# Performance work log

Measured on AMD Instinct MI355X. Metric: run time of the kernel, lower is better.

## Reference

```python
import jax, jax.numpy as jnp
import numpy as np

H = 256  # GRU hidden size


def _gru_scan(state, lengths, Wih, Whh, bih, bhh):
    # state: [B, T, D]; run a batched GRU over time, freezing h once t >= lengths[b]
    B, T, D = state.shape
    # precompute input gates for all timesteps: [T, B, 3H]
    gi_all = jnp.einsum('btd,gd->tbg', state, Wih) + bih

    def step(h, inp):
        gi, t = inp
        gh = h @ Whh.T + bhh                       # [B, 3H]
        i_r, i_z, i_n = jnp.split(gi, 3, axis=-1)
        h_r, h_z, h_n = jnp.split(gh, 3, axis=-1)
        r = jax.nn.sigmoid(i_r + h_r)
        z = jax.nn.sigmoid(i_z + h_z)
        n = jnp.tanh(i_n + r * h_n)
        h_new = (1.0 - z) * n + z * h              # torch GRUCell update
        mask = (t < lengths)[:, None]              # ragged: stop updating past length
        return jnp.where(mask, h_new, h), None

    h0 = jnp.zeros((B, H), state.dtype)
    h, _ = jax.lax.scan(step, h0, (gi_all, jnp.arange(T)))
    return h  # [B, H] = hidden after lengths[b] GRU steps


def _mlp(x, w1, b1, w2, b2, w3, b3, w4, b4, wq, bq):
    x = jax.nn.relu(x @ w1.T + b1)
    x = jax.nn.relu(x @ w2.T + b2)
    x = jax.nn.relu(x @ w3.T + b3)
    x = jax.nn.relu(x @ w4.T + b4)
    return x @ wq.T + bq  # [B, 1]


def setup_inputs() -> dict:
    key = jax.random.key(0)
    ks = jax.random.split(key, 40)
    B, T, D, A = 2048, 64, 15, 1
    inp = {}
    inp['state'] = jax.random.normal(ks[0], (B, T, D), jnp.float32)
    inp['action'] = jax.random.normal(ks[1], (B, A), jnp.float32)
    inp['lengths'] = jax.random.randint(ks[2], (B,), 1, T + 1, jnp.int32)
    i = 3
    for t in (1, 2):
        for name, shape, fan in [('Wih', (3 * H, D), D), ('Whh', (3 * H, H), H),
                                 ('bih', (3 * H,), H), ('bhh', (3 * H,), H)]:
            inp[f'g{t}_{name}'] = jax.random.normal(ks[i], shape, jnp.float32) / np.sqrt(fan)
            i += 1
        for name, (o, n) in [('fc1', (1024, H + D + A)), ('fc2', (1024, 1024)),
                             ('fc3', (512, 1024)), ('fc4', (256, 512)), ('q', (1, 256))]:
            inp[f'{name}_{t}_w'] = jax.random.normal(ks[i], (o, n), jnp.float32) / np.sqrt(n)
            i += 1
            inp[f'{name}_{t}_b'] = jax.random.normal(ks[i], (o,), jnp.float32) * 0.01
            i += 1
    return inp


def reference(state, action, lengths,
              g1_Wih, g1_Whh, g1_bih, g1_bhh,
              fc1_1_w, fc1_1_b, fc2_1_w, fc2_1_b, fc3_1_w, fc3_1_b,
              fc4_1_w, fc4_1_b, q_1_w, q_1_b,
              g2_Wih, g2_Whh, g2_bih, g2_bhh,
              fc1_2_w, fc1_2_b, fc2_2_w, fc2_2_b, fc3_2_w, fc3_2_b,
              fc4_2_w, fc4_2_b, q_2_w, q_2_b):
    h1 = _gru_scan(state, lengths, g1_Wih, g1_Whh, g1_bih, g1_bhh)
    h2 = _gru_scan(state, lengths, g2_Wih, g2_Whh, g2_bih, g2_bhh)
    aug = jnp.concatenate([state[:, 0, :], action], axis=-1)  # [B, 16]
    x1 = jnp.concatenate([aug, h1], axis=-1)                  # [B, 272]
    x2 = jnp.concatenate([aug, h2], axis=-1)
    out1 = _mlp(x1, fc1_1_w, fc1_1_b, fc2_1_w, fc2_1_b, fc3_1_w, fc3_1_b,
                fc4_1_w, fc4_1_b, q_1_w, q_1_b)
    out2 = _mlp(x2, fc1_2_w, fc1_2_b, fc2_2_w, fc2_2_b, fc3_2_w, fc3_2_b,
                fc4_2_w, fc4_2_b, q_2_w, q_2_b)
    return (out1, out2)
```

## Files before the change

kernel.cpp:

```cpp
#include <hip/hip_runtime.h>

typedef float  f32x4 __attribute__((ext_vector_type(4)));
typedef short  s16x8 __attribute__((ext_vector_type(8)));
typedef __bf16 b16x8 __attribute__((ext_vector_type(8)));

#define DEV __device__ __forceinline__

DEV unsigned short f2b(float f) {
  unsigned u = __builtin_bit_cast(unsigned, f);
  u = (u + 0x7FFFu + ((u >> 16) & 1u)) >> 16;
  return (unsigned short)u;
}
DEV b16x8 ld8(const unsigned short* p) {
  return __builtin_bit_cast(b16x8, *(const s16x8*)p);
}
DEV float sigm(float x) { return __builtin_amdgcn_rcpf(1.f + __expf(-x)); }
DEV float tanh_fast(float x) {
  float e = __expf(2.f * x);
  return 1.f - 2.f * __builtin_amdgcn_rcpf(e + 1.f);
}
DEV f32x4 mfma_bf16(b16x8 a, b16x8 b, f32x4 c) {
  return __builtin_amdgcn_mfma_f32_16x16x32_bf16(a, b, c, 0, 0, 0);
}

struct PrepArgs {
  const float *whh[2], *wih[2], *bih[2], *bhh[2];
  const float *src[2][4];
  unsigned short *waug[2], *dst[2][4];
  const float *qb[2];
  float *out;
};

__global__ __launch_bounds__(256) void prep_kernel(PrepArgs p) {
  const int job = blockIdx.y;
  const int i0 = blockIdx.x * 256 + threadIdx.x;
  const int stride = gridDim.x * 256;
  if (job < 2) {
    const float* whh = p.whh[job];
    const float* wih = p.wih[job];
    const float* bih = p.bih[job];
    const float* bhh = p.bhh[job];
    unsigned short* dst = p.waug[job];
    for (int idx = i0; idx < 768 * 288; idx += stride) {
      int j = idx / 288, k = idx - j * 288;
      float v = 0.f;
      if (k < 256) {
        int o = k & 31;
        int kk = (k & 0x1E0) + (o >> 1) + ((o & 1) << 4);
        v = whh[j * 256 + kk];
      } else if (k < 271)  v = wih[j * 15 + (k - 256)];
      else if (k == 271)   v = (j < 512) ? (bih[j] + bhh[j]) : bih[j];
      dst[idx] = f2b(v);
    }
  } else if (job < 10) {
    const int jj = job - 2, br = jj >> 2, ly = jj & 3;
    const int rowsA[4] = {1024, 1024, 512, 256};
    const int scA[4]   = {272, 1024, 1024, 512};
    const int dcA[4]   = {320, 1024, 1024, 512};
    const float* src = p.src[br][ly];
    unsigned short* dst = p.dst[br][ly];
    const int sc = scA[ly], dc = dcA[ly], tot = rowsA[ly] * dc;
    for (int idx = i0; idx < tot; idx += stride) {
      int r = idx / dc, c = idx - r * dc;
      float v = (c < sc) ? src[r * sc + c] : 0.f;
      dst[idx] = f2b(v);
    }
  } else {
    for (int idx = i0; idx < 4096; idx += stride)
      p.out[idx] = p.qb[idx >> 11][0];
  }
}

#define GRU_LDS_BYTES 147584
__attribute__((amdgpu_waves_per_eu(1, 1)))
__global__ void __launch_bounds__(256) gru_kernel(
    const float* __restrict__ state, const float* __restrict__ action,
    const int* __restrict__ lengths,
    const unsigned short* __restrict__ waug0, const unsigned short* __restrict__ waug1,
    const float* __restrict__ bhh0, const float* __restrict__ bhh1,
    unsigned short* __restrict__ x0, unsigned short* __restrict__ x1) {
  extern __shared__ char smem[];
  unsigned short* W7   = (unsigned short*)smem;
  unsigned short* WA   = (unsigned short*)(smem + 49152);
  unsigned short* SgL  = (unsigned short*)(smem + 98304);
  unsigned*       Hb2  = (unsigned*)(smem + 131072);
  int* lenS = (int*)(smem + 147456);
  int* mlS  = (int*)(smem + 147520);

  const int tid = threadIdx.x;
  const int lane = tid & 63, w = tid >> 6;
  const int l15 = lane & 15, q = lane >> 4;
  const int g = blockIdx.x & 1;
  const int r0 = (blockIdx.x >> 1) * 16;

  const unsigned short* Waug = g ? waug1 : waug0;
  const float* bhh = g ? bhh1 : bhh0;
  unsigned short* xout = g ? x1 : x0;

  for (int i = tid; i < 4096; i += 256) Hb2[i] = 0;
  if (tid < 16) lenS[tid] = lengths[r0 + tid];
  for (int s = tid; s < 64 * 32; s += 256) {
    const int t = s >> 5, L = s & 31;
    const int q2 = L >> 4, r = L & 15;
    const float* sp = state + (size_t)(r0 + r) * 960 + t * 15;
    s16x8 h;
#pragma unroll
    for (int j = 0; j < 8; j++) {
      const int k = q2 * 8 + j;
      float v = (k < 15) ? sp[k] : (k == 15 ? 1.0f : 0.f);
      h[j] = (short)f2b(v);
    }
    *(s16x8*)(SgL + (size_t)s * 8) = h;
  }
  __syncthreads();
  if (tid == 0) {
    int m = 1;
    for (int i = 0; i < 16; i++) m = lenS[i] > m ? lenS[i] : m;
    *mlS = m;
  }

  int c0[12];
#pragma unroll
  for (int gate = 0; gate < 3; gate++)
#pragma unroll
    for (int j = 0; j < 4; j++) c0[gate * 4 + j] = gate * 256 + 64 * w + 16 * j;

  b16x8 wres[12][7];
#pragma unroll
  for (int i = 0; i < 12; i++) {
    const unsigned short* bpi = Waug + (size_t)(c0[i] + l15) * 288 + q * 8;
#pragma unroll
    for (int j = 0; j < 7; j++) wres[i][j] = ld8(bpi + j * 32);
    *(s16x8*)(W7 + ((size_t)i * 256 + tid) * 8) =
        __builtin_bit_cast(s16x8, ld8(bpi + 7 * 32));
    *(s16x8*)(WA + ((size_t)i * 256 + tid) * 8) =
        __builtin_bit_cast(s16x8, ld8(bpi + 256));
  }
  float bnH[4];
#pragma unroll
  for (int j = 0; j < 4; j++) bnH[j] = bhh[c0[8 + j] + l15];
  int len4[4];
#pragma unroll
  for (int r = 0; r < 4; r++) len4[r] = lenS[q * 4 + r];

  int aOff[8];
#pragma unroll
  for (int k = 0; k < 8; k++) {
    const int ck = 4 * k + q;
    const int pk = (ck & 24) | ((ck & 7) ^ (l15 & 7));
    aOff[k] = l15 * 128 + pk * 4;
  }
  int wOff[2][4];
#pragma unroll
  for (int p = 0; p < 2; p++)
#pragma unroll
    for (int rg = 0; rg < 4; rg++) {
      const int row = q * 4 + rg;
      const int cb = 8 * w + 4 * p + (l15 >> 2);
      const int pw = (cb & 24) | ((cb & 7) ^ (row & 7));
      wOff[p][rg] = row * 128 + pw * 4 + (l15 & 3);
    }
  __syncthreads();
  const int maxlen = *mlS;

  float hold[4][4] = {{0,0,0,0},{0,0,0,0},{0,0,0,0},{0,0,0,0}};
  int poff = 0;

  for (int t = 0; t < maxlen; ++t) {
    __syncthreads();

    f32x4 acc[12];
#pragma unroll
    for (int i = 0; i < 12; i++) acc[i] = f32x4{0.f, 0.f, 0.f, 0.f};

    const unsigned* hb = Hb2 + poff;
    b16x8 a8 = ld8(SgL + t * 256 + ((q & 1) * 16 + l15) * 8);

#pragma unroll
    for (int k = 0; k < 7; k++) {
      b16x8 a = __builtin_bit_cast(b16x8, *(const uint4*)(hb + aOff[k]));
#pragma unroll
      for (int i = 0; i < 12; i++) acc[i] = mfma_bf16(a, wres[i][k], acc[i]);
    }
    {
      b16x8 a = __builtin_bit_cast(b16x8, *(const uint4*)(hb + aOff[7]));
#pragma unroll
      for (int i = 0; i < 12; i++) {
        b16x8 bw = ld8(W7 + ((size_t)i * 256 + tid) * 8);
        acc[i] = mfma_bf16(a, bw, acc[i]);
      }
    }
    f32x4 accNa[4];
#pragma unroll
    for (int i = 0; i < 8; i++) {
      b16x8 bw = ld8(WA + ((size_t)i * 256 + tid) * 8);
      acc[i] = mfma_bf16(a8, bw, acc[i]);
    }
#pragma unroll
    for (int j = 0; j < 4; j++) {
      b16x8 bw = ld8(WA + ((size_t)(8 + j) * 256 + tid) * 8);
      accNa[j] = mfma_bf16(a8, bw, f32x4{0.f, 0.f, 0.f, 0.f});
    }

    unsigned* hbw = Hb2 + (poff ^ 2048);
#pragma unroll
    for (int j = 0; j < 4; j++)
#pragma unroll
      for (int rg = 0; rg < 4; rg++) {
        const bool live = (t < len4[rg]);
        float inn = accNa[j][rg];
        float hn = acc[8 + j][rg] + bnH[j];
        float r = sigm(acc[j][rg]);
        float z = sigm(acc[4 + j][rg]);
        float n = tanh_fast(inn + r * hn);
        float h = n + z * (hold[j][rg] - n);
        h = live ? h : hold[j][rg];
        hold[j][rg] = h;
      }
#pragma unroll
    for (int p = 0; p < 2; p++)
#pragma unroll
      for (int rg = 0; rg < 4; rg++)
        hbw[wOff[p][rg]] = (unsigned)f2b(hold[2 * p][rg]) |
                           ((unsigned)f2b(hold[2 * p + 1][rg]) << 16);
    poff ^= 2048;
  }

#pragma unroll
  for (int j = 0; j < 4; j++)
#pragma unroll
    for (int rg = 0; rg < 4; rg++) {
      const int row = q * 4 + rg;
      xout[(size_t)(r0 + row) * 320 + 16 + c0[j] + l15] = f2b(hold[j][rg]);
    }
  for (int s = tid; s < 1024; s += 256) {
    const int row = s >> 6, cc = s & 63;
    float v; int col;
    if (cc < 15)       { v = state[(size_t)(r0 + row) * 960 + cc]; col = cc; }
    else if (cc == 15) { v = action[r0 + row]; col = 15; }
    else               { v = 0.f; col = 256 + cc; }
    xout[(size_t)(r0 + row) * 320 + col] = f2b(v);
  }
}

DEV int slotOf(int c) { return (c & ~7) | ((c & 7) ^ ((c >> 3) & 7)); }

__global__ __launch_bounds__(256, 4) void gemm_dbuf(
    const unsigned short* __restrict__ A0, const unsigned short* __restrict__ A1,
    const unsigned short* __restrict__ W0, const unsigned short* __restrict__ W1,
    const float* __restrict__ b0, const float* __restrict__ b1,
    unsigned short* __restrict__ Y0, unsigned short* __restrict__ Y1,
    int N, int K) {
  const unsigned short* A = blockIdx.z ? A1 : A0;
  const unsigned short* W = blockIdx.z ? W1 : W0;
  const float* bias = blockIdx.z ? b1 : b0;
  unsigned short* Y = blockIdx.z ? Y1 : Y0;

  const int tid = threadIdx.x;
  const int lane = tid & 63, wid = tid >> 6;
  const int wm = wid >> 1, wn = wid & 1;
  const int l15 = lane & 15, q = lane >> 4;
  const int m0 = blockIdx.x * 64, n0 = blockIdx.y * 64;

  __shared__ unsigned short As[2][4096];
  __shared__ unsigned short Bs[2][4096];

  f32x4 acc[2][2];
#pragma unroll
  for (int mi = 0; mi < 2; mi++)
#pragma unroll
    for (int ni = 0; ni < 2; ni++) acc[mi][ni] = f32x4{0.f, 0.f, 0.f, 0.f};

  const int c0c = tid * 2, c1c = tid * 2 + 1;
  const int ar0 = c0c >> 3, ak0 = (c0c & 7) * 8;
  const int ar1 = c1c >> 3, ak1 = (c1c & 7) * 8;
  const int ws0 = slotOf(c0c) * 8, ws1 = slotOf(c1c) * 8;
  const unsigned short* pa0 = A + (size_t)(m0 + ar0) * K + ak0;
  const unsigned short* pa1 = A + (size_t)(m0 + ar1) * K + ak1;
  const unsigned short* pb0 = W + (size_t)(n0 + ar0) * K + ak0;
  const unsigned short* pb1 = W + (size_t)(n0 + ar1) * K + ak1;

  const int niter = K >> 6;
  s16x8 ra0 = *(const s16x8*)pa0, ra1 = *(const s16x8*)pa1;
  s16x8 rb0 = *(const s16x8*)pb0, rb1 = *(const s16x8*)pb1;
  *(s16x8*)&As[0][ws0] = ra0; *(s16x8*)&As[0][ws1] = ra1;
  *(s16x8*)&Bs[0][ws0] = rb0; *(s16x8*)&Bs[0][ws1] = rb1;

  for (int it = 0; it < niter; ++it) {
    const unsigned short* as = As[it & 1];
    const unsigned short* bs = Bs[it & 1];
    const bool pf = (it + 1 < niter);
    if (pf) {
      const int k0 = (it + 1) << 6;
      ra0 = *(const s16x8*)(pa0 + k0); ra1 = *(const s16x8*)(pa1 + k0);
      rb0 = *(const s16x8*)(pb0 + k0); rb1 = *(const s16x8*)(pb1 + k0);
    }
    __syncthreads();

#pragma unroll
    for (int s = 0; s < 2; s++) {
      b16x8 af[2], bf[2];
#pragma unroll
      for (int mi = 0; mi < 2; mi++) {
        const int ml = wm * 32 + mi * 16 + l15;
        af[mi] = ld8(as + slotOf(ml * 8 + s * 4 + q) * 8);
      }
#pragma unroll
      for (int ni = 0; ni < 2; ni++) {
        const int nl = wn * 32 + ni * 16 + l15;
        bf[ni] = ld8(bs + slotOf(nl * 8 + s * 4 + q) * 8);
      }
#pragma unroll
      for (int mi = 0; mi < 2; mi++)
#pragma unroll
        for (int ni = 0; ni < 2; ni++)
          acc[mi][ni] = mfma_bf16(af[mi], bf[ni], acc[mi][ni]);
    }
    if (pf) {
      const int nb = (it + 1) & 1;
      *(s16x8*)&As[nb][ws0] = ra0; *(s16x8*)&As[nb][ws1] = ra1;
      *(s16x8*)&Bs[nb][ws0] = rb0; *(s16x8*)&Bs[nb][ws1] = rb1;
    }
  }

#pragma unroll
  for (int ni = 0; ni < 2; ni++) {
    const int col = n0 + wn * 32 + ni * 16 + l15;
    const float bv = bias[col];
#pragma unroll
    for (int mi = 0; mi < 2; mi++) {
      const int rbase = m0 + wm * 32 + mi * 16 + q * 4;
#pragma unroll
      for (int rg = 0; rg < 4; rg++) {
        float v = acc[mi][ni][rg] + bv;
        v = fmaxf(v, 0.f);
        Y[(size_t)(rbase + rg) * N + col] = f2b(v);
      }
    }
  }
}

DEV void async16(const unsigned short* g, unsigned short* l) {
  __builtin_amdgcn_global_load_lds(
      (const __attribute__((address_space(1))) unsigned int*)g,
      (__attribute__((address_space(3))) unsigned int*)l, 16, 0, 0);
}

__global__ __launch_bounds__(256, 4) void fc4q_kernel(
    const unsigned short* __restrict__ A0, const unsigned short* __restrict__ A1,
    const unsigned short* __restrict__ W0, const unsigned short* __restrict__ W1,
    const float* __restrict__ b0, const float* __restrict__ b1,
    const float* __restrict__ qw0, const float* __restrict__ qw1,
    float* __restrict__ out) {
  const unsigned short* A = blockIdx.z ? A1 : A0;
  const unsigned short* W = blockIdx.z ? W1 : W0;
  const float* bias = blockIdx.z ? b1 : b0;
  const float* qw = blockIdx.z ? qw1 : qw0;

  const int tid = threadIdx.x;
  const int lane = tid & 63, wn = tid >> 6;
  const int l15 = lane & 15, q = lane >> 4;
  const int m0 = blockIdx.x * 32;
  const int nbase = blockIdx.y * 128;
  const int K = 512;

  __shared__ unsigned short As[32 * 32];
  __shared__ unsigned short Bs[128 * 32];
  __shared__ float red[32][4];

  f32x4 acc[2][2];
#pragma unroll
  for (int mi = 0; mi < 2; mi++)
#pragma unroll
    for (int ni = 0; ni < 2; ni++) acc[mi][ni] = f32x4{0.f, 0.f, 0.f, 0.f};

  const int srow = tid >> 2, scol = (tid & 3) * 8;
  for (int k0 = 0; k0 < K; k0 += 32) {
    if (tid < 128)
      async16(A + (size_t)(m0 + srow) * K + scol + k0, &As[tid * 8]);
#pragma unroll
    for (int g64 = 0; g64 < 2; g64++)
      async16(W + (size_t)(nbase + g64 * 64 + srow) * K + scol + k0,
              &Bs[g64 * 2048 + tid * 8]);
    __syncthreads();

    b16x8 af[2], bf[2];
#pragma unroll
    for (int mi = 0; mi < 2; mi++)
      af[mi] = ld8(&As[(mi * 16 + l15) * 32 + q * 8]);
#pragma unroll
    for (int ni = 0; ni < 2; ni++)
      bf[ni] = ld8(&Bs[(wn * 32 + ni * 16 + l15) * 32 + q * 8]);
#pragma unroll
    for (int mi = 0; mi < 2; mi++)
#pragma unroll
      for (int ni = 0; ni < 2; ni++)
        acc[mi][ni] = mfma_bf16(af[mi], bf[ni], acc[mi][ni]);
    __syncthreads();
  }

#pragma unroll
  for (int mi = 0; mi < 2; mi++) {
#pragma unroll
    for (int rg = 0; rg < 4; rg++) {
      float s = 0.f;
#pragma unroll
      for (int ni = 0; ni < 2; ni++) {
        const int col = nbase + wn * 32 + ni * 16 + l15;
        float v = fmaxf(acc[mi][ni][rg] + bias[col], 0.f);
        s += v * qw[col];
      }
#pragma unroll
      for (int off = 1; off < 16; off <<= 1) s += __shfl_xor(s, off);
      if (l15 == 0) red[mi * 16 + q * 4 + rg][wn] = s;
    }
  }
  __syncthreads();
  if (tid < 32) {
    float t = red[tid][0] + red[tid][1] + red[tid][2] + red[tid][3];
    atomicAdd(out + (size_t)blockIdx.z * 2048 + m0 + tid, t);
  }
}

extern "C" void kernel_launch(void* const* d_in, const int* in_sizes, int n_in,
                              void* d_out, int out_size, void* d_ws, size_t ws_size,
                              hipStream_t stream) {
  const float* state   = (const float*)d_in[0];
  const float* action  = (const float*)d_in[1];
  const int*   lengths = (const int*)d_in[2];
  const float* g_wih[2] = {(const float*)d_in[3], (const float*)d_in[17]};
  const float* g_whh[2] = {(const float*)d_in[4], (const float*)d_in[18]};
  const float* g_bih[2] = {(const float*)d_in[5], (const float*)d_in[19]};
  const float* g_bhh[2] = {(const float*)d_in[6], (const float*)d_in[20]};
  const float* fcw[2][4] = {
      {(const float*)d_in[7], (const float*)d_in[9], (const float*)d_in[11], (const float*)d_in[13]},
      {(const float*)d_in[21], (const float*)d_in[23], (const float*)d_in[25], (const float*)d_in[27]}};
  const float* fcb[2][4] = {
      {(const float*)d_in[8], (const float*)d_in[10], (const float*)d_in[12], (const float*)d_in[14]},
      {(const float*)d_in[22], (const float*)d_in[24], (const float*)d_in[26], (const float*)d_in[28]}};
  const float* qw[2] = {(const float*)d_in[15], (const float*)d_in[29]};
  const float* qb[2] = {(const float*)d_in[16], (const float*)d_in[30]};
  float* out = (float*)d_out;

  uintptr_t base = (uintptr_t)d_ws;
  auto alloc = [&](size_t bytes) -> unsigned short* {
    void* p = (void*)base;
    base += (bytes + 255) & ~(size_t)255;
    return (unsigned short*)p;
  };
  unsigned short *waug[2], *w1b[2], *w2b[2], *w3b[2], *w4b[2], *xb[2], *yA[2], *yB[2];
  for (int g = 0; g < 2; g++) waug[g] = alloc(768 * 288 * 2);
  for (int g = 0; g < 2; g++) w1b[g] = alloc(1024 * 320 * 2);
  for (int g = 0; g < 2; g++) w2b[g] = alloc(1024 * 1024 * 2);
  for (int g = 0; g < 2; g++) w3b[g] = alloc(512 * 1024 * 2);
  for (int g = 0; g < 2; g++) w4b[g] = alloc(256 * 512 * 2);
  for (int g = 0; g < 2; g++) xb[g] = alloc(2048 * 320 * 2);
  for (int g = 0; g < 2; g++) yA[g] = alloc(2048 * 1024 * 2);
  for (int g = 0; g < 2; g++) yB[g] = alloc(2048 * 1024 * 2);
  (void)ws_size; (void)in_sizes; (void)n_in; (void)out_size;

  PrepArgs pa;
  for (int g = 0; g < 2; g++) {
    pa.whh[g] = g_whh[g]; pa.wih[g] = g_wih[g];
    pa.bih[g] = g_bih[g]; pa.bhh[g] = g_bhh[g];
    pa.waug[g] = waug[g];
    pa.src[g][0] = fcw[g][0]; pa.dst[g][0] = w1b[g];
    pa.src[g][1] = fcw[g][1]; pa.dst[g][1] = w2b[g];
    pa.src[g][2] = fcw[g][2]; pa.dst[g][2] = w3b[g];
    pa.src[g][3] = fcw[g][3]; pa.dst[g][3] = w4b[g];
    pa.qb[g] = qb[g];
  }
  pa.out = out;
  prep_kernel<<<dim3(64, 11), 256, 0, stream>>>(pa);

  (void)hipFuncSetAttribute((const void*)gru_kernel,
                            hipFuncAttributeMaxDynamicSharedMemorySize,
                            GRU_LDS_BYTES);
  gru_kernel<<<dim3(256), dim3(256), GRU_LDS_BYTES, stream>>>(
      state, action, lengths, waug[0], waug[1], g_bhh[0], g_bhh[1], xb[0], xb[1]);

  gemm_dbuf<<<dim3(32, 16, 2), 256, 0, stream>>>(
      xb[0], xb[1], w1b[0], w1b[1], fcb[0][0], fcb[1][0], yA[0], yA[1], 1024, 320);
  gemm_dbuf<<<dim3(32, 16, 2), 256, 0, stream>>>(
      yA[0], yA[1], w2b[0], w2b[1], fcb[0][1], fcb[1][1], yB[0], yB[1], 1024, 1024);
  gemm_dbuf<<<dim3(32, 8, 2), 256, 0, stream>>>(
      yB[0], yB[1], w3b[0], w3b[1], fcb[0][2], fcb[1][2], yA[0], yA[1], 512, 1024);
  fc4q_kernel<<<dim3(64, 2, 2), 256, 0, stream>>>(
      yA[0], yA[1], w4b[0], w4b[1], fcb[0][3], fcb[1][3], qw[0], qw[1], out);
}
```

Measured before the change: 360.8 us.

## Split GRU recurrence across 8 waves with partial register/global/LDS weight residency

The GRU kernel now runs with 512 threads (8 waves) per 16-row block, so each wave owns 32 hidden columns instead of 64. Recurrent weights are split three ways: 4 k-slices stay in registers, 3 are streamed from global/L2 every step with software prefetch, and 2 live in LDS. Biases are folded into accumulator initialisation, and the hidden state uses a single padded LDS buffer with an extra barrier instead of a swizzled double buffer. The goal is more waves to hide MFMA and transcendental latency. The cost is extra per-step global weight traffic and an additional sync each timestep.

```diff
diff --git a/kernel.cpp b/kernel.cpp
--- a/kernel.cpp
+++ b/kernel.cpp
@@ -19,12 +19,17 @@
   float e = __expf(2.f * x);
   return 1.f - 2.f * __builtin_amdgcn_rcpf(e + 1.f);
 }
+DEV void async16(const unsigned short* g, unsigned short* l) {
+  __builtin_amdgcn_global_load_lds(
+      (const __attribute__((address_space(1))) unsigned int*)g,
+      (__attribute__((address_space(3))) unsigned int*)l, 16, 0, 0);
+}
 DEV f32x4 mfma_bf16(b16x8 a, b16x8 b, f32x4 c) {
   return __builtin_amdgcn_mfma_f32_16x16x32_bf16(a, b, c, 0, 0, 0);
 }
 
 struct PrepArgs {
-  const float *whh[2], *wih[2], *bih[2], *bhh[2];
+  const float *whh[2], *wih[2];
   const float *src[2][4];
   unsigned short *waug[2], *dst[2][4];
   const float *qb[2];
@@ -38,18 +43,12 @@
   if (job < 2) {
     const float* whh = p.whh[job];
     const float* wih = p.wih[job];
-    const float* bih = p.bih[job];
-    const float* bhh = p.bhh[job];
     unsigned short* dst = p.waug[job];
     for (int idx = i0; idx < 768 * 288; idx += stride) {
       int j = idx / 288, k = idx - j * 288;
       float v = 0.f;
-      if (k < 256) {
-        int o = k & 31;
-        int kk = (k & 0x1E0) + (o >> 1) + ((o & 1) << 4);
-        v = whh[j * 256 + kk];
-      } else if (k < 271)  v = wih[j * 15 + (k - 256)];
-      else if (k == 271)   v = (j < 512) ? (bih[j] + bhh[j]) : bih[j];
+      if (k < 256)      v = whh[j * 256 + k];
+      else if (k < 271) v = wih[j * 15 + (k - 256)];
       dst[idx] = f2b(v);
     }
   } else if (job < 10) {
@@ -71,21 +70,21 @@
   }
 }
 
-#define GRU_LDS_BYTES 147584
-__attribute__((amdgpu_waves_per_eu(1, 1)))
-__global__ void __launch_bounds__(256) gru_kernel(
+#define GRU_LDS_BYTES 140672
+__global__ __launch_bounds__(512) void gru_kernel(
     const float* __restrict__ state, const float* __restrict__ action,
     const int* __restrict__ lengths,
     const unsigned short* __restrict__ waug0, const unsigned short* __restrict__ waug1,
-    const float* __restrict__ bhh0, const float* __restrict__ bhh1,
+    const float* __restrict__ bih0, const float* __restrict__ bhh0,
+    const float* __restrict__ bih1, const float* __restrict__ bhh1,
     unsigned short* __restrict__ x0, unsigned short* __restrict__ x1) {
   extern __shared__ char smem[];
-  unsigned short* W7   = (unsigned short*)smem;
-  unsigned short* WA   = (unsigned short*)(smem + 49152);
+  unsigned short* W67L = (unsigned short*)smem;
   unsigned short* SgL  = (unsigned short*)(smem + 98304);
-  unsigned*       Hb2  = (unsigned*)(smem + 131072);
-  int* lenS = (int*)(smem + 147456);
-  int* mlS  = (int*)(smem + 147520);
+  unsigned short* Hb   = (unsigned short*)(smem + 131072);
+  int* lenS = (int*)(smem + 140544);
+  int* mlS  = (int*)(smem + 140608);
+  float* tmpF = (float*)smem;
 
   const int tid = threadIdx.x;
   const int lane = tid & 63, w = tid >> 6;
@@ -94,24 +93,17 @@
   const int r0 = (blockIdx.x >> 1) * 16;
 
   const unsigned short* Waug = g ? waug1 : waug0;
+  const float* bih = g ? bih1 : bih0;
   const float* bhh = g ? bhh1 : bhh0;
   unsigned short* xout = g ? x1 : x0;
 
-  for (int i = tid; i < 4096; i += 256) Hb2[i] = 0;
+  {
+    const float4* src = (const float4*)(state + (size_t)r0 * 960);
+    float4* dstv = (float4*)tmpF;
+    for (int i = tid; i < 3840; i += 512) dstv[i] = src[i];
+  }
+  for (int i = tid; i < 16 * 296; i += 512) Hb[i] = 0;
   if (tid < 16) lenS[tid] = lengths[r0 + tid];
-  for (int s = tid; s < 64 * 32; s += 256) {
-    const int t = s >> 5, L = s & 31;
-    const int q2 = L >> 4, r = L & 15;
-    const float* sp = state + (size_t)(r0 + r) * 960 + t * 15;
-    s16x8 h;
-#pragma unroll
-    for (int j = 0; j < 8; j++) {
-      const int k = q2 * 8 + j;
-      float v = (k < 15) ? sp[k] : (k == 15 ? 1.0f : 0.f);
-      h[j] = (short)f2b(v);
-    }
-    *(s16x8*)(SgL + (size_t)s * 8) = h;
-  }
   __syncthreads();
   if (tid == 0) {
     int m = 1;
@@ -119,121 +111,143 @@
     *mlS = m;
   }
 
-  int c0[12];
-#pragma unroll
-  for (int gate = 0; gate < 3; gate++)
-#pragma unroll
-    for (int j = 0; j < 4; j++) c0[gate * 4 + j] = gate * 256 + 64 * w + 16 * j;
-
-  b16x8 wres[12][7];
-#pragma unroll
-  for (int i = 0; i < 12; i++) {
-    const unsigned short* bpi = Waug + (size_t)(c0[i] + l15) * 288 + q * 8;
-#pragma unroll
-    for (int j = 0; j < 7; j++) wres[i][j] = ld8(bpi + j * 32);
-    *(s16x8*)(W7 + ((size_t)i * 256 + tid) * 8) =
-        __builtin_bit_cast(s16x8, ld8(bpi + 7 * 32));
-    *(s16x8*)(WA + ((size_t)i * 256 + tid) * 8) =
-        __builtin_bit_cast(s16x8, ld8(bpi + 256));
-  }
-  float bnH[4];
-#pragma unroll
-  for (int j = 0; j < 4; j++) bnH[j] = bhh[c0[8 + j] + l15];
+  for (int s = tid; s < 64 * 32; s += 512) {
+    const int t = s >> 5, L = s & 31;
+    const int q2 = L >> 4, r = L & 15;
+    s16x8 h;
+#pragma unroll
+    for (int j = 0; j < 8; j++) {
+      const int k = q2 * 8 + j;
+      float v = (k < 15) ? tmpF[r * 960 + t * 15 + k] : (k == 15 ? 1.0f : 0.f);
+      h[j] = (short)f2b(v);
+    }
+    *(s16x8*)(SgL + (size_t)s * 8) = h;
+  }
+  __syncthreads();
+
+  int c0[6];
+  c0[0] = 32 * w;       c0[1] = 32 * w + 16;
+  c0[2] = 256 + 32 * w; c0[3] = 256 + 32 * w + 16;
+  c0[4] = 512 + 32 * w; c0[5] = 512 + 32 * w + 16;
+
+  float brz[4];
+#pragma unroll
+  for (int i = 0; i < 4; i++) brz[i] = bih[c0[i] + l15] + bhh[c0[i] + l15];
+  float bnI[2] = {bih[c0[4] + l15], bih[c0[5] + l15]};
+  float bnH[2] = {bhh[c0[4] + l15], bhh[c0[5] + l15]};
+
+  const unsigned short* bp[6];
+#pragma unroll
+  for (int i = 0; i < 6; i++) bp[i] = Waug + (size_t)(c0[i] + l15) * 288 + q * 8;
+
+  b16x8 wres[6][4];
+  const int ksmap[4] = {8, 0, 1, 2};
+#pragma unroll
+  for (int i = 0; i < 6; i++) {
+#pragma unroll
+    for (int j = 0; j < 4; j++) wres[i][j] = ld8(bp[i] + ksmap[j] * 32);
+#pragma unroll
+    for (int ks2 = 0; ks2 < 2; ks2++) {
+      b16x8 v = ld8(bp[i] + (6 + ks2) * 32);
+      *(s16x8*)(W67L + (size_t)(ks2 * 6 + i) * 4096 + tid * 8) =
+          __builtin_bit_cast(s16x8, v);
+    }
+  }
   int len4[4];
 #pragma unroll
   for (int r = 0; r < 4; r++) len4[r] = lenS[q * 4 + r];
-
-  int aOff[8];
-#pragma unroll
-  for (int k = 0; k < 8; k++) {
-    const int ck = 4 * k + q;
-    const int pk = (ck & 24) | ((ck & 7) ^ (l15 & 7));
-    aOff[k] = l15 * 128 + pk * 4;
-  }
-  int wOff[2][4];
-#pragma unroll
-  for (int p = 0; p < 2; p++)
+  __syncthreads();
+  const int maxlen = *mlS;
+
+  float hold[2][4] = {{0, 0, 0, 0}, {0, 0, 0, 0}};
+  const short qmask = (q < 2) ? (short)-1 : (short)0;
+  const s16x8 qm = {qmask, qmask, qmask, qmask, qmask, qmask, qmask, qmask};
+
+  for (int t = 0; t < maxlen; ++t) {
+    __syncthreads();
+
+    f32x4 acc[6];
+#pragma unroll
+    for (int i = 0; i < 4; i++) acc[i] = f32x4{brz[i], brz[i], brz[i], brz[i]};
+    acc[4] = f32x4{bnI[0], bnI[0], bnI[0], bnI[0]};
+    acc[5] = f32x4{bnI[1], bnI[1], bnI[1], bnI[1]};
+
+    {
+      s16x8 raw = *(const s16x8*)(SgL + t * 256 + ((q & 1) * 16 + l15) * 8);
+      raw &= qm;
+      b16x8 a8 = __builtin_bit_cast(b16x8, raw);
+#pragma unroll
+      for (int i = 0; i < 6; i++) acc[i] = mfma_bf16(a8, wres[i][0], acc[i]);
+    }
+    f32x4 giN0 = acc[4], giN1 = acc[5];
+    acc[4] = acc[4] + bnH[0];
+    acc[5] = acc[5] + bnH[1];
+
+#pragma unroll
+    for (int j = 1; j < 4; j++) {
+      b16x8 a = ld8(&Hb[l15 * 296 + (j - 1) * 32 + q * 8]);
+#pragma unroll
+      for (int i = 0; i < 6; i++) acc[i] = mfma_bf16(a, wres[i][j], acc[i]);
+    }
+
+    b16x8 bs[6];
+#pragma unroll
+    for (int i = 0; i < 6; i++) bs[i] = ld8(bp[i] + 3 * 32);
+#pragma unroll
+    for (int ks = 3; ks <= 5; ++ks) {
+      b16x8 cur[6];
+#pragma unroll
+      for (int i = 0; i < 6; i++) cur[i] = bs[i];
+      if (ks < 5) {
+#pragma unroll
+        for (int i = 0; i < 6; i++) bs[i] = ld8(bp[i] + (ks + 1) * 32);
+      }
+      b16x8 a = ld8(&Hb[l15 * 296 + ks * 32 + q * 8]);
+#pragma unroll
+      for (int i = 0; i < 6; i++) acc[i] = mfma_bf16(a, cur[i], acc[i]);
+    }
+
+#pragma unroll
+    for (int ks2 = 0; ks2 < 2; ks2++) {
+      b16x8 a = ld8(&Hb[l15 * 296 + (6 + ks2) * 32 + q * 8]);
+#pragma unroll
+      for (int i = 0; i < 6; i++) {
+        b16x8 bw = ld8(W67L + (size_t)(ks2 * 6 + i) * 4096 + tid * 8);
+        acc[i] = mfma_bf16(a, bw, acc[i]);
+      }
+    }
+
+    __syncthreads();
+
+#pragma unroll
+    for (int i = 0; i < 2; i++) {
+      const int c = 32 * w + 16 * i + l15;
+#pragma unroll
+      for (int rg = 0; rg < 4; rg++) {
+        const int row = q * 4 + rg;
+        float r = sigm(acc[0 + i][rg]);
+        float z = sigm(acc[2 + i][rg]);
+        float inn = i ? giN1[rg] : giN0[rg];
+        float hn = acc[4 + i][rg] - inn;
+        float nn = tanh_fast(inn + r * hn);
+        float hv = (1.f - z) * nn + z * hold[i][rg];
+        hv = (t < len4[rg]) ? hv : hold[i][rg];
+        hold[i][rg] = hv;
+        Hb[row * 296 + c] = f2b(hv);
+      }
+    }
+  }
+
+#pragma unroll
+  for (int i = 0; i < 2; i++) {
+    const int c = 32 * w + 16 * i + l15;
 #pragma unroll
     for (int rg = 0; rg < 4; rg++) {
       const int row = q * 4 + rg;
-      const int cb = 8 * w + 4 * p + (l15 >> 2);
-      const int pw = (cb & 24) | ((cb & 7) ^ (row & 7));
-      wOff[p][rg] = row * 128 + pw * 4 + (l15 & 3);
-    }
-  __syncthreads();
-  const int maxlen = *mlS;
-
-  float hold[4][4] = {{0,0,0,0},{0,0,0,0},{0,0,0,0},{0,0,0,0}};
-  int poff = 0;
-
-  for (int t = 0; t < maxlen; ++t) {
-    __syncthreads();
-
-    f32x4 acc[12];
-#pragma unroll
-    for (int i = 0; i < 12; i++) acc[i] = f32x4{0.f, 0.f, 0.f, 0.f};
-
-    const unsigned* hb = Hb2 + poff;
-    b16x8 a8 = ld8(SgL + t * 256 + ((q & 1) * 16 + l15) * 8);
-
-#pragma unroll
-    for (int k = 0; k < 7; k++) {
-      b16x8 a = __builtin_bit_cast(b16x8, *(const uint4*)(hb + aOff[k]));
-#pragma unroll
-      for (int i = 0; i < 12; i++) acc[i] = mfma_bf16(a, wres[i][k], acc[i]);
-    }
-    {
-      b16x8 a = __builtin_bit_cast(b16x8, *(const uint4*)(hb + aOff[7]));
-#pragma unroll
-      for (int i = 0; i < 12; i++) {
-        b16x8 bw = ld8(W7 + ((size_t)i * 256 + tid) * 8);
-        acc[i] = mfma_bf16(a, bw, acc[i]);
-      }
-    }
-    f32x4 accNa[4];
-#pragma unroll
-    for (int i = 0; i < 8; i++) {
-      b16x8 bw = ld8(WA + ((size_t)i * 256 + tid) * 8);
-      acc[i] = mfma_bf16(a8, bw, acc[i]);
-    }
-#pragma unroll
-    for (int j = 0; j < 4; j++) {
-      b16x8 bw = ld8(WA + ((size_t)(8 + j) * 256 + tid) * 8);
-      accNa[j] = mfma_bf16(a8, bw, f32x4{0.f, 0.f, 0.f, 0.f});
-    }
-
-    unsigned* hbw = Hb2 + (poff ^ 2048);
-#pragma unroll
-    for (int j = 0; j < 4; j++)
-#pragma unroll
-      for (int rg = 0; rg < 4; rg++) {
-        const bool live = (t < len4[rg]);
-        float inn = accNa[j][rg];
-        float hn = acc[8 + j][rg] + bnH[j];
-        float r = sigm(acc[j][rg]);
-        float z = sigm(acc[4 + j][rg]);
-        float n = tanh_fast(inn + r * hn);
-        float h = n + z * (hold[j][rg] - n);
-        h = live ? h : hold[j][rg];
-        hold[j][rg] = h;
-      }
-#pragma unroll
-    for (int p = 0; p < 2; p++)
-#pragma unroll
-      for (int rg = 0; rg < 4; rg++)
-        hbw[wOff[p][rg]] = (unsigned)f2b(hold[2 * p][rg]) |
-                           ((unsigned)f2b(hold[2 * p + 1][rg]) << 16);
-    poff ^= 2048;
-  }
-
-#pragma unroll
-  for (int j = 0; j < 4; j++)
-#pragma unroll
-    for (int rg = 0; rg < 4; rg++) {
-      const int row = q * 4 + rg;
-      xout[(size_t)(r0 + row) * 320 + 16 + c0[j] + l15] = f2b(hold[j][rg]);
-    }
-  for (int s = tid; s < 1024; s += 256) {
+      xout[(size_t)(r0 + row) * 320 + 16 + c] = f2b(hold[i][rg]);
+    }
+  }
+  for (int s = tid; s < 1024; s += 512) {
     const int row = s >> 6, cc = s & 63;
     float v; int col;
     if (cc < 15)       { v = state[(size_t)(r0 + row) * 960 + cc]; col = cc; }
@@ -338,12 +352,6 @@
       }
     }
   }
-}
-
-DEV void async16(const unsigned short* g, unsigned short* l) {
-  __builtin_amdgcn_global_load_lds(
-      (const __attribute__((address_space(1))) unsigned int*)g,
-      (__attribute__((address_space(3))) unsigned int*)l, 16, 0, 0);
 }
 
 __global__ __launch_bounds__(256, 4) void fc4q_kernel(
@@ -462,7 +470,6 @@
   PrepArgs pa;
   for (int g = 0; g < 2; g++) {
     pa.whh[g] = g_whh[g]; pa.wih[g] = g_wih[g];
-    pa.bih[g] = g_bih[g]; pa.bhh[g] = g_bhh[g];
     pa.waug[g] = waug[g];
     pa.src[g][0] = fcw[g][0]; pa.dst[g][0] = w1b[g];
     pa.src[g][1] = fcw[g][1]; pa.dst[g][1] = w2b[g];
@@ -476,8 +483,9 @@
   (void)hipFuncSetAttribute((const void*)gru_kernel,
                             hipFuncAttributeMaxDynamicSharedMemorySize,
                             GRU_LDS_BYTES);
-  gru_kernel<<<dim3(256), dim3(256), GRU_LDS_BYTES, stream>>>(
-      state, action, lengths, waug[0], waug[1], g_bhh[0], g_bhh[1], xb[0], xb[1]);
+  gru_kernel<<<dim3(256), dim3(512), GRU_LDS_BYTES, stream>>>(
+      state, action, lengths, waug[0], waug[1],
+      g_bih[0], g_bhh[0], g_bih[1], g_bhh[1], xb[0], xb[1]);
 
   gemm_dbuf<<<dim3(32, 16, 2), 256, 0, stream>>>(
       xb[0], xb[1], w1b[0], w1b[1], fcb[0][0], fcb[1][0], yA[0], yA[1], 1024, 320);
```

Result: faster. 339.0 us (-6.0%).
